# Optimization experiments

Hardware: AMD Instinct MI355X
Metric: run time of the kernel (lower is better)

## Reference

```python
import jax, jax.numpy as jnp
import numpy as np

B, V = 256, 2048
PD, MD, H = 1024, 512, 512

def setup_inputs() -> dict:
    key = jax.random.key(0)
    k1, k2, k3, k4, k5 = jax.random.split(key, 5)
    patient_emb = jax.random.normal(k1, (B, PD), dtype=jnp.float32)
    atc4_emb = jax.random.normal(k2, (V, MD), dtype=jnp.float32)
    # Linear(PD+MD -> H): weight (H, PD+MD), bias (H,)
    W1 = jax.random.normal(k3, (H, PD + MD), dtype=jnp.float32) * 0.02
    b1 = jnp.zeros((H,), dtype=jnp.float32)
    # Linear(H -> 1): weight (1, H) -> store as (H,), bias scalar
    w2 = jax.random.normal(k4, (H,), dtype=jnp.float32) * 0.05
    b2 = jnp.zeros((), dtype=jnp.float32)
    return {"patient_emb": patient_emb, "atc4_emb": atc4_emb,
            "W1": W1, "b1": b1, "w2": w2, "b2": b2}

def reference(patient_emb, atc4_emb, W1, b1, w2, b2):
    # Algebraically equivalent to cat([patient, mol]) @ W1.T:
    # split W1 into patient and mol blocks, matmul each, broadcast-add.
    W1p = W1[:, :PD]   # (H, PD)
    W1m = W1[:, PD:]   # (H, MD)
    hp = jnp.einsum('bp,hp->bh', patient_emb, W1p)   # (B, H)
    hm = jnp.einsum('vm,hm->vh', atc4_emb, W1m)      # (V, H)
    h = jnp.tanh(hp[:, None, :] + hm[None, :, :] + b1)  # (B, V, H)
    scores = jnp.einsum('bvh,h->bv', h, w2) + b2     # (B, V)
    return scores
```

## Files before the change

kernel.cpp:

```cpp
#include <hip/hip_runtime.h>
#include <hip/hip_bf16.h>
#include <math.h>

typedef __attribute__((ext_vector_type(8))) short short8;
typedef __attribute__((ext_vector_type(4))) float float4v;
typedef __attribute__((ext_vector_type(2))) float float2v;

__device__ __forceinline__ int2 cvt2bf16x4(float4v v) {
    union { __hip_bfloat162 h2; int i; } u0, u1;
    u0.h2 = __float22bfloat162_rn(make_float2(v.x, v.y));
    u1.h2 = __float22bfloat162_rn(make_float2(v.z, v.w));
    return make_int2(u0.i, u1.i);
}

__global__ __launch_bounds__(256, 2) void gemm_exp(
    const float* __restrict__ patient, const float* __restrict__ atc4,
    const float* __restrict__ W1, const float* __restrict__ b1,
    float* __restrict__ EA, float* __restrict__ EM)
{
    const float* A; const float* W; const float* bias; float* T;
    int lda, K, M;
    int bx = blockIdx.x;
    if (bx < 4) {
        A = patient; lda = 1024; K = 1024; M = 256; bias = b1; T = EA; W = W1;
    } else {
        bx -= 4;
        A = atc4;    lda = 512;  K = 512;  M = 2048; bias = nullptr; T = EM; W = W1 + 1024;
    }
    const int ldw = 1536;

    __shared__ short As[64][72];
    __shared__ short Bs[64][72];
    const int t = threadIdx.x;
    const int m0 = bx * 64;
    const int n0 = blockIdx.y * 64;
    const int wave = t >> 6;
    const int lane = t & 63;
    const int wm = (wave & 1) * 32;
    const int wn = (wave >> 1) * 32;
    const int lrow = lane & 15;
    const int quad = lane >> 4;

    float4v acc[2][2];
    #pragma unroll
    for (int i = 0; i < 2; i++)
        #pragma unroll
        for (int j = 0; j < 2; j++)
            acc[i][j] = (float4v){0.f, 0.f, 0.f, 0.f};

    const int sr = t >> 2;
    const int sc = (t & 3) * 16;

    float4v av[4], wv[4];
    {
        const float* ap = A + (size_t)(m0 + sr) * lda + sc;
        const float* wp = W + (size_t)(n0 + sr) * ldw + sc;
        #pragma unroll
        for (int ii = 0; ii < 4; ii++) {
            av[ii] = *(const float4v*)(ap + ii * 4);
            wv[ii] = *(const float4v*)(wp + ii * 4);
        }
    }

    for (int k0 = 0; k0 < K; k0 += 64) {
        #pragma unroll
        for (int ii = 0; ii < 4; ii++) {
            *(int2*)&As[sr][sc + ii * 4] = cvt2bf16x4(av[ii]);
            *(int2*)&Bs[sr][sc + ii * 4] = cvt2bf16x4(wv[ii]);
        }
        __syncthreads();
        if (k0 + 64 < K) {
            const float* ap = A + (size_t)(m0 + sr) * lda + (k0 + 64 + sc);
            const float* wp = W + (size_t)(n0 + sr) * ldw + (k0 + 64 + sc);
            #pragma unroll
            for (int ii = 0; ii < 4; ii++) {
                av[ii] = *(const float4v*)(ap + ii * 4);
                wv[ii] = *(const float4v*)(wp + ii * 4);
            }
        }
        #pragma unroll
        for (int kk = 0; kk < 64; kk += 32) {
            short8 af[2], bfr[2];
            #pragma unroll
            for (int i = 0; i < 2; i++)
                af[i] = *(const short8*)&As[wm + i * 16 + lrow][kk + quad * 8];
            #pragma unroll
            for (int j = 0; j < 2; j++)
                bfr[j] = *(const short8*)&Bs[wn + j * 16 + lrow][kk + quad * 8];
            #pragma unroll
            for (int i = 0; i < 2; i++)
                #pragma unroll
                for (int j = 0; j < 2; j++)
                    acc[i][j] = __builtin_amdgcn_mfma_f32_16x16x32_bf16(
                        af[i], bfr[j], acc[i][j], 0, 0, 0);
        }
        __syncthreads();
    }

    #pragma unroll
    for (int i = 0; i < 2; i++) {
        #pragma unroll
        for (int j = 0; j < 2; j++) {
            const int n  = n0 + wn + j * 16 + lrow;
            const int mb = m0 + wm + i * 16 + quad * 4;
            const float bn = bias ? bias[n] : 0.0f;
            float4v ev;
            #pragma unroll
            for (int r = 0; r < 4; r++)
                ev[r] = __expf(2.0f * (acc[i][j][r] + bn));
            *(float4v*)&T[(size_t)n * M + mb] = ev;
        }
    }
}

__device__ __forceinline__ float4v splat4(float x) {
    return (float4v){x, x, x, x};
}

__global__ __launch_bounds__(256, 4) void pair_kernel(
    const float* __restrict__ EA, const float* __restrict__ EM,
    const float* __restrict__ w2, float* __restrict__ partial)
{
    __shared__ float sEA[64][68];
    __shared__ float sEM[64][68];
    __shared__ float4v sC4[16];
    const int t  = threadIdx.x;
    const int v0 = blockIdx.x * 64;
    const int b0 = blockIdx.y * 64;
    const int h0 = blockIdx.z * 64;
    const int tx = t & 15;
    const int ty = t >> 4;

    if (t < 16) {
        float4v wvq = *(const float4v*)(w2 + h0 + 4 * t);
        sC4[t] = -2.0f * wvq;
    }

    float4v acc[4];
    #pragma unroll
    for (int i = 0; i < 4; i++)
        acc[i] = (float4v){0.f, 0.f, 0.f, 0.f};

    {
        const int rS = t >> 2;
        const int c0i = (t & 3) * 16;
        const float* pa = EA + (size_t)(h0 + rS) * 256 + b0 + c0i;
        const float* pm = EM + (size_t)(h0 + rS) * 2048 + v0 + c0i;
        #pragma unroll
        for (int i = 0; i < 4; i++) {
            float4v va = *(const float4v*)(pa + 4 * i);
            float4v vm = *(const float4v*)(pm + 4 * i);
            *(float4v*)&sEA[rS][c0i + 4 * i] = va;
            *(float4v*)&sEM[rS][c0i + 4 * i] = vm;
        }
    }
    __syncthreads();

    const float4v one4 = {1.f, 1.f, 1.f, 1.f};

    #pragma unroll 1
    for (int q = 0; q < 16; q++) {
        const int hq = 4 * q;
        const float4v m0 = *(const float4v*)&sEM[hq    ][tx * 4];
        const float4v m1 = *(const float4v*)&sEM[hq + 1][tx * 4];
        const float4v m2 = *(const float4v*)&sEM[hq + 2][tx * 4];
        const float4v m3 = *(const float4v*)&sEM[hq + 3][tx * 4];
        const float4v ea0 = *(const float4v*)&sEA[hq    ][ty * 4];
        const float4v ea1 = *(const float4v*)&sEA[hq + 1][ty * 4];
        const float4v ea2 = *(const float4v*)&sEA[hq + 2][ty * 4];
        const float4v ea3 = *(const float4v*)&sEA[hq + 3][ty * 4];
        const float4v c = sC4[q];
        const float4v c0 = splat4(c.x);
        const float4v c1 = splat4(c.y);
        const float4v c2 = splat4(c.z);
        const float4v c3 = splat4(c.w);
        #pragma unroll
        for (int i = 0; i < 4; i++) {
            const float4v d0 = __builtin_elementwise_fma(m0, splat4(ea0[i]), one4);
            const float4v d1 = __builtin_elementwise_fma(m1, splat4(ea1[i]), one4);
            const float4v d2 = __builtin_elementwise_fma(m2, splat4(ea2[i]), one4);
            const float4v d3 = __builtin_elementwise_fma(m3, splat4(ea3[i]), one4);
            const float4v e01 = d0 * d1;
            const float4v e23 = d2 * d3;
            const float4v n01 = __builtin_elementwise_fma(d1, c0, d0 * c1);
            const float4v n23 = __builtin_elementwise_fma(d3, c2, d2 * c3);
            const float4v num = __builtin_elementwise_fma(n01, e23, n23 * e01);
            const float4v den = e01 * e23;
            const float4v r = { __builtin_amdgcn_rcpf(den.x),
                                __builtin_amdgcn_rcpf(den.y),
                                __builtin_amdgcn_rcpf(den.z),
                                __builtin_amdgcn_rcpf(den.w) };
            acc[i] = __builtin_elementwise_fma(num, r, acc[i]);
        }
    }

    float4v w2q = sC4[0];
    #pragma unroll
    for (int k = 1; k < 16; k++) w2q += sC4[k];
    const float w2s = -0.5f * (w2q.x + w2q.y + w2q.z + w2q.w);
    const float4v w2s4 = splat4(w2s);

    const size_t pb = (size_t)blockIdx.z * (256 * 2048);
    #pragma unroll
    for (int i = 0; i < 4; i++) {
        const size_t row = pb + (size_t)(b0 + ty * 4 + i) * 2048 + v0 + tx * 4;
        float4v o = acc[i] + w2s4;
        *(float4v*)&partial[row] = o;
    }
}

__global__ __launch_bounds__(256) void reduce_kernel(
    const float* __restrict__ partial, const float* __restrict__ b2,
    float* __restrict__ out)
{
    const int i = (blockIdx.x * 256 + threadIdx.x) * 4;
    const float bb = b2[0];
    float4v s = *(const float4v*)&partial[i];
    #pragma unroll
    for (int z = 1; z < 8; z++)
        s += *(const float4v*)&partial[(size_t)z * 524288 + i];
    float4v o = s + bb;
    *(float4v*)&out[i] = o;
}

extern "C" void kernel_launch(void* const* d_in, const int* in_sizes, int n_in,
                              void* d_out, int out_size, void* d_ws, size_t ws_size,
                              hipStream_t stream)
{
    const float* patient = (const float*)d_in[0];
    const float* atc4    = (const float*)d_in[1];
    const float* W1      = (const float*)d_in[2];
    const float* b1      = (const float*)d_in[3];
    const float* w2      = (const float*)d_in[4];
    const float* b2      = (const float*)d_in[5];
    float* out = (float*)d_out;
    float* ws  = (float*)d_ws;

    float* EA      = ws;
    float* EM      = ws + 131072;
    float* partial = ws + 1179648;

    gemm_exp<<<dim3(36, 8, 1), 256, 0, stream>>>(patient, atc4, W1, b1, EA, EM);
    pair_kernel<<<dim3(32, 4, 8), 256, 0, stream>>>(EA, EM, w2, partial);
    reduce_kernel<<<512, 256, 0, stream>>>(partial, b2, out);
}
```

Baseline: 111.6 us.

## Halve pair-kernel batch tile and stream H in 16-row chunks for occupancy

The pair kernel's batch tile drops from 64 to 32 rows per block, doubling the grid. The full 64-row H slab is no longer staged once; it is now loaded in four 16-row chunks with a sync before and after each. This cuts shared memory and registers per block so the launch bound can rise to 6 blocks per CU. In exchange there are more barriers, less reuse of each EM element per load, and each block does less work.

```diff
diff --git a/kernel.cpp b/kernel.cpp
--- a/kernel.cpp
+++ b/kernel.cpp
@@ -117,16 +117,16 @@
     return (float4v){x, x, x, x};
 }
 
-__global__ __launch_bounds__(256, 4) void pair_kernel(
+__global__ __launch_bounds__(256, 6) void pair_kernel(
     const float* __restrict__ EA, const float* __restrict__ EM,
     const float* __restrict__ w2, float* __restrict__ partial)
 {
-    __shared__ float sEA[64][68];
-    __shared__ float sEM[64][68];
+    __shared__ float sEA[16][36];
+    __shared__ float sEM[16][68];
     __shared__ float4v sC4[16];
     const int t  = threadIdx.x;
     const int v0 = blockIdx.x * 64;
-    const int b0 = blockIdx.y * 64;
+    const int b0 = blockIdx.y * 32;
     const int h0 = blockIdx.z * 64;
     const int tx = t & 15;
     const int ty = t >> 4;
@@ -136,61 +136,60 @@
         sC4[t] = -2.0f * wvq;
     }
 
-    float4v acc[4];
-    #pragma unroll
-    for (int i = 0; i < 4; i++)
-        acc[i] = (float4v){0.f, 0.f, 0.f, 0.f};
-
-    {
-        const int rS = t >> 2;
-        const int c0i = (t & 3) * 16;
-        const float* pa = EA + (size_t)(h0 + rS) * 256 + b0 + c0i;
-        const float* pm = EM + (size_t)(h0 + rS) * 2048 + v0 + c0i;
-        #pragma unroll
-        for (int i = 0; i < 4; i++) {
-            float4v va = *(const float4v*)(pa + 4 * i);
-            float4v vm = *(const float4v*)(pm + 4 * i);
-            *(float4v*)&sEA[rS][c0i + 4 * i] = va;
-            *(float4v*)&sEM[rS][c0i + 4 * i] = vm;
-        }
-    }
-    __syncthreads();
-
+    float4v acc[2];
+    acc[0] = (float4v){0.f, 0.f, 0.f, 0.f};
+    acc[1] = (float4v){0.f, 0.f, 0.f, 0.f};
+
+    const int rSt = t >> 4;
+    const int cq  = t & 15;
     const float4v one4 = {1.f, 1.f, 1.f, 1.f};
 
     #pragma unroll 1
-    for (int q = 0; q < 16; q++) {
-        const int hq = 4 * q;
-        const float4v m0 = *(const float4v*)&sEM[hq    ][tx * 4];
-        const float4v m1 = *(const float4v*)&sEM[hq + 1][tx * 4];
-        const float4v m2 = *(const float4v*)&sEM[hq + 2][tx * 4];
-        const float4v m3 = *(const float4v*)&sEM[hq + 3][tx * 4];
-        const float4v ea0 = *(const float4v*)&sEA[hq    ][ty * 4];
-        const float4v ea1 = *(const float4v*)&sEA[hq + 1][ty * 4];
-        const float4v ea2 = *(const float4v*)&sEA[hq + 2][ty * 4];
-        const float4v ea3 = *(const float4v*)&sEA[hq + 3][ty * 4];
-        const float4v c = sC4[q];
-        const float4v c0 = splat4(c.x);
-        const float4v c1 = splat4(c.y);
-        const float4v c2 = splat4(c.z);
-        const float4v c3 = splat4(c.w);
-        #pragma unroll
-        for (int i = 0; i < 4; i++) {
-            const float4v d0 = __builtin_elementwise_fma(m0, splat4(ea0[i]), one4);
-            const float4v d1 = __builtin_elementwise_fma(m1, splat4(ea1[i]), one4);
-            const float4v d2 = __builtin_elementwise_fma(m2, splat4(ea2[i]), one4);
-            const float4v d3 = __builtin_elementwise_fma(m3, splat4(ea3[i]), one4);
-            const float4v e01 = d0 * d1;
-            const float4v e23 = d2 * d3;
-            const float4v n01 = __builtin_elementwise_fma(d1, c0, d0 * c1);
-            const float4v n23 = __builtin_elementwise_fma(d3, c2, d2 * c3);
-            const float4v num = __builtin_elementwise_fma(n01, e23, n23 * e01);
-            const float4v den = e01 * e23;
-            const float4v r = { __builtin_amdgcn_rcpf(den.x),
-                                __builtin_amdgcn_rcpf(den.y),
-                                __builtin_amdgcn_rcpf(den.z),
-                                __builtin_amdgcn_rcpf(den.w) };
-            acc[i] = __builtin_elementwise_fma(num, r, acc[i]);
+    for (int s = 0; s < 4; s++) {
+        __syncthreads();
+        {
+            const size_t hr = (size_t)(h0 + s * 16 + rSt);
+            float4v vm = *(const float4v*)(EM + hr * 2048 + v0 + cq * 4);
+            float2v va = *(const float2v*)(EA + hr * 256  + b0 + cq * 2);
+            *(float4v*)&sEM[rSt][cq * 4] = vm;
+            *(float2v*)&sEA[rSt][cq * 2] = va;
+        }
+        __syncthreads();
+
+        #pragma unroll
+        for (int q = 0; q < 4; q++) {
+            const int hr = 4 * q;
+            const float4v m0 = *(const float4v*)&sEM[hr    ][tx * 4];
+            const float4v m1 = *(const float4v*)&sEM[hr + 1][tx * 4];
+            const float4v m2 = *(const float4v*)&sEM[hr + 2][tx * 4];
+            const float4v m3 = *(const float4v*)&sEM[hr + 3][tx * 4];
+            const float2v ea0 = *(const float2v*)&sEA[hr    ][ty * 2];
+            const float2v ea1 = *(const float2v*)&sEA[hr + 1][ty * 2];
+            const float2v ea2 = *(const float2v*)&sEA[hr + 2][ty * 2];
+            const float2v ea3 = *(const float2v*)&sEA[hr + 3][ty * 2];
+            const float4v c = sC4[s * 4 + q];
+            const float4v c0 = splat4(c.x);
+            const float4v c1 = splat4(c.y);
+            const float4v c2 = splat4(c.z);
+            const float4v c3 = splat4(c.w);
+            #pragma unroll
+            for (int i = 0; i < 2; i++) {
+                const float4v d0 = __builtin_elementwise_fma(m0, splat4(ea0[i]), one4);
+                const float4v d1 = __builtin_elementwise_fma(m1, splat4(ea1[i]), one4);
+                const float4v d2 = __builtin_elementwise_fma(m2, splat4(ea2[i]), one4);
+                const float4v d3 = __builtin_elementwise_fma(m3, splat4(ea3[i]), one4);
+                const float4v e01 = d0 * d1;
+                const float4v e23 = d2 * d3;
+                const float4v n01 = __builtin_elementwise_fma(d1, c0, d0 * c1);
+                const float4v n23 = __builtin_elementwise_fma(d3, c2, d2 * c3);
+                const float4v num = __builtin_elementwise_fma(n01, e23, n23 * e01);
+                const float4v den = e01 * e23;
+                const float4v r = { __builtin_amdgcn_rcpf(den.x),
+                                    __builtin_amdgcn_rcpf(den.y),
+                                    __builtin_amdgcn_rcpf(den.z),
+                                    __builtin_amdgcn_rcpf(den.w) };
+                acc[i] = __builtin_elementwise_fma(num, r, acc[i]);
+            }
         }
     }
 
@@ -202,8 +201,8 @@
 
     const size_t pb = (size_t)blockIdx.z * (256 * 2048);
     #pragma unroll
-    for (int i = 0; i < 4; i++) {
-        const size_t row = pb + (size_t)(b0 + ty * 4 + i) * 2048 + v0 + tx * 4;
+    for (int i = 0; i < 2; i++) {
+        const size_t row = pb + (size_t)(b0 + ty * 2 + i) * 2048 + v0 + tx * 4;
         float4v o = acc[i] + w2s4;
         *(float4v*)&partial[row] = o;
     }
@@ -241,6 +240,6 @@
     float* partial = ws + 1179648;
 
     gemm_exp<<<dim3(36, 8, 1), 256, 0, stream>>>(patient, atc4, W1, b1, EA, EM);
-    pair_kernel<<<dim3(32, 4, 8), 256, 0, stream>>>(EA, EM, w2, partial);
+    pair_kernel<<<dim3(32, 8, 8), 256, 0, stream>>>(EA, EM, w2, partial);
     reduce_kernel<<<512, 256, 0, stream>>>(partial, b2, out);
 }
```

After: 113.0 us. About the same (+1.3%).
